# Kernel tuning notes

Measured on AMD Instinct MI355X. Metric: run time of the kernel, lower is better.

Reference implementation:

```python
import jax, jax.numpy as jnp
import numpy as np

EPS = 1e-5
NEG_SLOPE = 0.2  # torch LeakyReLU default in DGCNN-style SharedMLPs


def knn_idx(p, k):
    # p: [B, 3, N]; returns idx [B, N, k] of k nearest neighbors (incl. self)
    inner = jnp.einsum('bdn,bdm->bnm', p, p)           # [B,N,N]
    sq = jnp.sum(p * p, axis=1)                         # [B,N]
    neg_dist = 2.0 * inner - sq[:, :, None] - sq[:, None, :]
    return jax.lax.top_k(neg_dist, k)[1]                # [B,N,k]


def smlp1d(x, w, b, g, bt):
    # x: [B,C,N]; 1x1 conv + BatchNorm1d (batch stats) + LeakyReLU
    y = jnp.einsum('bcn,oc->bon', x, w) + b[None, :, None]
    m = y.mean(axis=(0, 2), keepdims=True)
    v = y.var(axis=(0, 2), keepdims=True)
    y = g[None, :, None] * (y - m) * jax.lax.rsqrt(v + EPS) + bt[None, :, None]
    return jax.nn.leaky_relu(y, NEG_SLOPE)


def edgeconv(x, idx, w, b, g, bt):
    # x: [B,C,N], idx: [B,N,k] -> [B,O,N]
    B = x.shape[0]
    xT = jnp.transpose(x, (0, 2, 1))                    # [B,N,C]
    nb = xT[jnp.arange(B)[:, None, None], idx]          # [B,N,k,C] gather
    ctr = jnp.broadcast_to(xT[:, :, None, :], nb.shape)
    feat = jnp.concatenate([nb - ctr, ctr], axis=-1)    # [B,N,k,2C]
    y = jnp.einsum('bnkc,oc->bnko', feat, w) + b        # 1x1 conv2d
    m = y.mean(axis=(0, 1, 2), keepdims=True)
    v = y.var(axis=(0, 1, 2), keepdims=True)
    y = g * (y - m) * jax.lax.rsqrt(v + EPS) + bt
    y = jax.nn.leaky_relu(y, NEG_SLOPE)
    y = jnp.max(y, axis=2)                              # max over k -> [B,N,O]
    return jnp.transpose(y, (0, 2, 1))                  # [B,O,N]


def setup_inputs() -> dict:
    key = jax.random.key(0)
    ks = jax.random.split(key, 16)
    B, N, K = 2, 8192, 20
    C_in = 1024 + 3 * 64  # emb_dims + n_edgeconvs_backbone*64 = 1216
    OUT = 50

    def lin(k, o, c):
        return jax.random.normal(k, (o, c), jnp.float32) * (1.0 / np.sqrt(c))

    return {
        'x': jax.random.normal(ks[0], (B, C_in, N), jnp.float32),
        'p': jax.random.normal(ks[1], (B, 3, N), jnp.float32),
        # smlp1: 1216 -> 256
        'w1': lin(ks[2], 256, C_in), 'b1': jnp.zeros((256,), jnp.float32),
        'g1': jnp.ones((256,), jnp.float32), 'bt1': jnp.zeros((256,), jnp.float32),
        # edgeconv: 512 -> 256
        'we': lin(ks[3], 256, 512), 'be': jnp.zeros((256,), jnp.float32),
        'ge': jnp.ones((256,), jnp.float32), 'bte': jnp.zeros((256,), jnp.float32),
        # smlp2 part 1: 256 -> 256
        'w2': lin(ks[4], 256, 256), 'b2': jnp.zeros((256,), jnp.float32),
        'g2': jnp.ones((256,), jnp.float32), 'bt2': jnp.zeros((256,), jnp.float32),
        # smlp2 part 2: 256 -> 128
        'w3': lin(ks[5], 128, 256), 'b3': jnp.zeros((128,), jnp.float32),
        'g3': jnp.ones((128,), jnp.float32), 'bt3': jnp.zeros((128,), jnp.float32),
        # final conv1d: 128 -> 50
        'wf': lin(ks[6], OUT, 128), 'bf': jnp.zeros((OUT,), jnp.float32),
    }


def reference(x, p, w1, b1, g1, bt1, we, be, ge, bte,
              w2, b2, g2, bt2, w3, b3, g3, bt3, wf, bf):
    K = 20
    h = smlp1d(x, w1, b1, g1, bt1)              # [B,256,N]
    idx = knn_idx(p, K)                          # [B,N,K]
    h = edgeconv(h, idx, we, be, ge, bte)        # [B,256,N]
    h = smlp1d(h, w2, b2, g2, bt2)               # Dropout2d: identity (eval)
    h = smlp1d(h, w3, b3, g3, bt3)               # [B,128,N]
    return jnp.einsum('bcn,oc->bon', h, wf) + bf[None, :, None]  # [B,50,N]
```

## Files before the change

kernel.cpp:

```cpp
#include <hip/hip_runtime.h>

typedef unsigned short u16;
typedef unsigned int   u32;
typedef unsigned long long u64;
typedef __attribute__((ext_vector_type(4))) float f4;
typedef __attribute__((ext_vector_type(8))) short s8;
typedef __attribute__((ext_vector_type(4))) int   i4v;
typedef __attribute__((ext_vector_type(4))) unsigned short u16x4;

#define DEV __device__ __forceinline__

DEV u16 f2b(float f) {
  u32 u = __float_as_uint(f);
  return (u16)((u + 0x7FFFu + ((u >> 16) & 1u)) >> 16);
}
DEV float b2f(u16 h) { return __uint_as_float(((u32)h) << 16); }

#define OFF_STATS 0L
#define OFF_W1B   65536L
#define OFF_WEAB  688128L
#define OFF_W2B   950272L
#define OFF_W3B   1081344L
#define OFF_IDX   1146880L
#define OFF_PQ    2457600L
#define OFF_XT    4194304L
#define OFF_Y1    44040192L
#define OFF_Y2    4194304L
#define OFF_EMAX  23068672L
#define OFF_EMIN  41943040L
#define OFF_Y3    4194304L
#define OFF_Y4    23068672L
#define WS_NEED   71303168L

__global__ __launch_bounds__(256) void k_convw(
    const float* __restrict__ w1, const float* __restrict__ we,
    const float* __restrict__ w2, const float* __restrict__ w3,
    u16* __restrict__ w1b, u16* __restrict__ weABb,
    u16* __restrict__ w2b, u16* __restrict__ w3b)
{
  int i = blockIdx.x * 256 + threadIdx.x;
  if (i < 311296) { w1b[i] = f2b(w1[i]); return; }
  i -= 311296;
  if (i < 131072) {
    int o = i >> 8, c = i & 255;
    float v = (o < 256) ? we[o * 512 + c]
                        : we[(o - 256) * 512 + 256 + c] - we[(o - 256) * 512 + c];
    weABb[i] = f2b(v); return;
  }
  i -= 131072;
  if (i < 65536) { w2b[i] = f2b(w2[i]); return; }
  i -= 65536;
  if (i < 32768) { w3b[i] = f2b(w3[i]); }
}

__global__ __launch_bounds__(256) void k_prep(const float* __restrict__ p, f4* __restrict__ pqg)
{
  int i = blockIdx.x * 256 + threadIdx.x;
  int b = i >> 13, n = i & 8191;
  const float* pb = p + (long)b * 24576;
  float X = pb[n], Y = pb[8192 + n], Z = pb[16384 + n];
  f4 v; v[0] = X; v[1] = Y; v[2] = Z; v[3] = fmaf(X, X, fmaf(Y, Y, Z * Z));
  pqg[i] = v;
}

__global__ __launch_bounds__(256) void k_xt(const float* __restrict__ x, u16* __restrict__ xt)
{
  __shared__ float t[64][65];
  const int b = blockIdx.z, ct = blockIdx.y, nt = blockIdx.x;
  const int tx = threadIdx.x & 63, ty = threadIdx.x >> 6;
  const float* xb = x + (long)b * 1216 * 8192;
#pragma unroll
  for (int i = 0; i < 16; ++i) {
    int c = ct * 64 + ty + i * 4;
    t[ty + i * 4][tx] = xb[(long)c * 8192 + nt * 64 + tx];
  }
  __syncthreads();
  u16* xtb = xt + (long)b * 8192 * 1216;
#pragma unroll
  for (int i = 0; i < 16; ++i) {
    int n = nt * 64 + ty + i * 4;
    xtb[(long)n * 1216 + ct * 64 + tx] = f2b(t[tx][ty + i * 4]);
  }
}

__global__ __launch_bounds__(256) void k_knn(const f4* __restrict__ pqg, int* __restrict__ idxOut)
{
  __shared__ f4 chunk[1024];
  __shared__ u16 cand[4][4][128];
  __shared__ double ckeyv[4][128];
  __shared__ int scnt[4][4];
  const int tid = threadIdx.x, lane = tid & 63, w = tid >> 6;
  const int blk = blockIdx.x;
  const int b = blk >> 9;
  const int qbase = ((blk & 511) << 4) + (w << 2);
  const f4* __restrict__ P = pqg + ((long)b << 13);
  if (lane < 4) scnt[w][lane] = 0;
  float qx2[4], qy2[4], qz2[4];
#pragma unroll
  for (int j = 0; j < 4; ++j) {
    f4 Q = P[qbase + j];
    qx2[j] = Q[0] + Q[0]; qy2[j] = Q[1] + Q[1]; qz2[j] = Q[2] + Q[2];
  }
  float mx[4];
#pragma unroll
  for (int j = 0; j < 4; ++j) mx[j] = -3.0e38f;
  for (int c = 0; c < 8; ++c) {
    __syncthreads();
#pragma unroll
    for (int i = 0; i < 4; ++i) chunk[tid + i * 256] = P[c * 1024 + tid + i * 256];
    __syncthreads();
#pragma unroll 2
    for (int t = 0; t < 16; ++t) {
      f4 cc = chunk[(t << 6) + lane];
#pragma unroll
      for (int j = 0; j < 4; ++j) {
        float v = fmaf(qx2[j], cc[0], fmaf(qy2[j], cc[1], fmaf(qz2[j], cc[2], -cc[3])));
        mx[j] = fmaxf(mx[j], v);
      }
    }
  }
  float sv[4];
#pragma unroll
  for (int j = 0; j < 4; ++j) sv[j] = mx[j];
#pragma unroll
  for (int k = 2; k <= 64; k <<= 1) {
#pragma unroll
    for (int s = k >> 1; s > 0; s >>= 1) {
      const bool takeMin = (((lane & k) == 0) == ((lane & s) == 0));
#pragma unroll
      for (int j = 0; j < 4; ++j) {
        float o = __shfl_xor(sv[j], s);
        sv[j] = takeMin ? fminf(sv[j], o) : fmaxf(sv[j], o);
      }
    }
  }
  float T[4];
#pragma unroll
  for (int j = 0; j < 4; ++j) T[j] = __shfl(sv[j], 44) - 1e-3f;
  for (int c = 0; c < 8; ++c) {
    __syncthreads();
#pragma unroll
    for (int i = 0; i < 4; ++i) chunk[tid + i * 256] = P[c * 1024 + tid + i * 256];
    __syncthreads();
#pragma unroll 2
    for (int t = 0; t < 16; ++t) {
      f4 cc = chunk[(t << 6) + lane];
#pragma unroll
      for (int j = 0; j < 4; ++j) {
        float v = fmaf(qx2[j], cc[0], fmaf(qy2[j], cc[1], fmaf(qz2[j], cc[2], -cc[3])));
        if (v >= T[j]) {
          int pos = atomicAdd(&scnt[w][j], 1);
          if (pos < 128) cand[w][j][pos] = (u16)(c * 1024 + (t << 6) + lane);
        }
      }
    }
  }
  asm volatile("s_waitcnt lgkmcnt(0)" ::: "memory");
  for (int j = 0; j < 4; ++j) {
    int cn = scnt[w][j]; if (cn > 128) cn = 128;
    f4 Q = P[qbase + j];
    const double Qx = (double)Q[0], Qy = (double)Q[1], Qz = (double)Q[2];
    const double Qs = Qx * Qx + Qy * Qy + Qz * Qz;
    double myV[2]; int myI[2];
#pragma unroll
    for (int jj = 0; jj < 2; ++jj) {
      const int e = lane + (jj << 6);
      myV[jj] = -1.0e300; myI[jj] = 0x7FFFFFFF;
      if (e < cn) {
        const int ci = cand[w][j][e];
        f4 c = P[ci];
        double cx = (double)c[0], cy = (double)c[1], cz = (double)c[2];
        double v = 2.0 * (Qx * cx + Qy * cy + Qz * cz) - Qs - (cx * cx + cy * cy + cz * cz);
        myV[jj] = v; myI[jj] = ci;
        ckeyv[w][e] = v;
      }
    }
    asm volatile("s_waitcnt lgkmcnt(0)" ::: "memory");
    int rk0 = 0, rk1 = 0;
#pragma unroll 4
    for (int e2 = 0; e2 < cn; ++e2) {
      double ov = ckeyv[w][e2];
      int oi = (int)cand[w][j][e2];
      rk0 += ((ov > myV[0]) || (ov == myV[0] && oi < myI[0])) ? 1 : 0;
      rk1 += ((ov > myV[1]) || (ov == myV[1] && oi < myI[1])) ? 1 : 0;
    }
    int* orow = idxOut + (((long)b << 13) + qbase + j) * 20;
    if (lane < cn && rk0 < 20) orow[rk0] = myI[0];
    if (lane + 64 < cn && rk1 < 20) orow[rk1] = myI[1];
    asm volatile("s_waitcnt lgkmcnt(0)" ::: "memory");
  }
}

DEV float lky(float z) { return z > 0.f ? z : 0.2f * z; }

DEV i4v applyPack8(f4 a, f4 b4, const float* sc, const float* sh, int kb) {
  u16 r[8];
#pragma unroll
  for (int e = 0; e < 4; ++e) r[e] = f2b(lky(fmaf(sc[kb + e], a[e], sh[kb + e])));
#pragma unroll
  for (int e = 0; e < 4; ++e) r[4 + e] = f2b(lky(fmaf(sc[kb + 4 + e], b4[e], sh[kb + 4 + e])));
  i4v o;
#pragma unroll
  for (int e = 0; e < 4; ++e) o[e] = (int)((u32)r[2 * e] | ((u32)r[2 * e + 1] << 16));
  return o;
}

DEV i4v selPack8b(i4v rawM, i4v rawN, const float* sc, const float* sh, int kb) {
  u16 r[8];
#pragma unroll
  for (int e = 0; e < 8; ++e) {
    u32 dM = (u32)rawM[e >> 1], dN = (u32)rawN[e >> 1];
    u16 hM = (e & 1) ? (u16)(dM >> 16) : (u16)(dM & 0xFFFFu);
    u16 hN = (e & 1) ? (u16)(dN >> 16) : (u16)(dN & 0xFFFFu);
    float s = sc[kb + e];
    float y = (s >= 0.f) ? b2f(hM) : b2f(hN);
    r[e] = f2b(lky(fmaf(s, y, sh[kb + e])));
  }
  i4v o;
#pragma unroll
  for (int e = 0; e < 4; ++e) o[e] = (int)((u32)r[2 * e] | ((u32)r[2 * e + 1] << 16));
  return o;
}

template<int BMODE, int STATS, int BF16OUT>
__global__ __launch_bounds__(256, 2) void k_gemm(
    const u16* __restrict__ A, const void* __restrict__ B0v, const void* __restrict__ B1v,
    const float* __restrict__ sums, const float* __restrict__ ssq,
    const float* __restrict__ g, const float* __restrict__ bt, float invCount,
    float* __restrict__ gsums, float* __restrict__ gssq,
    void* __restrict__ Yv, int M, int K, long strideB, long strideY)
{
  __shared__ u16 sA[2][4096];
  __shared__ u16 sB[2][4096];
  __shared__ float scB[256], shB[256];
  __shared__ float s_sum[128], s_ssq[128];
  const int b = blockIdx.z;
  const int m0 = blockIdx.y * 128;
  const int n0 = blockIdx.x * 128;
  const int tid = threadIdx.x, lane = tid & 63, w = tid >> 6;
  const int wr = w >> 1, wc = w & 1;
  const int r15 = lane & 15, g8 = (lane >> 4) * 8;

  if (BMODE != 0) {
    float m = sums[tid] * invCount;
    float v = ssq[tid] * invCount - m * m;
    float s = g[tid] / sqrtf(v + 1e-5f);
    scB[tid] = s;
    shB[tid] = bt[tid] - m * s;
  }
  if (STATS) { if (tid < 128) { s_sum[tid] = 0.f; s_ssq[tid] = 0.f; } }
  if (BMODE != 0) __syncthreads();

  f4 acc[4][4];
#pragma unroll
  for (int i = 0; i < 4; ++i)
#pragma unroll
    for (int j = 0; j < 4; ++j) { f4 z = {0.f, 0.f, 0.f, 0.f}; acc[i][j] = z; }

  const int row0 = tid >> 2;
  const int kp0 = (tid & 3) << 3;
  const u16* gA0 = A + (long)(m0 + row0) * K + kp0;
  const u16* gA1 = A + (long)(m0 + row0 + 64) * K + kp0;
  const int ch0 = tid, ch1 = tid + 256;

  const u16* gB0 = (const u16*)B0v + (long)b * strideB + (long)(n0 + row0) * K + kp0;
  const u16* gB1 = gB0 + (long)64 * K;
  const float* fB0 = (const float*)B0v + (long)b * strideB + (long)(n0 + row0) * K + kp0;
  const float* fB1 = fB0 + (long)64 * K;
  const u16* nB0 = (const u16*)B1v + (long)b * strideB + (long)(n0 + row0) * K + kp0;
  const u16* nB1 = nB0 + (long)64 * K;

  ((i4v*)sA[0])[ch0] = *(const i4v*)gA0;
  ((i4v*)sA[0])[ch1] = *(const i4v*)gA1;
  if (BMODE == 0) {
    ((i4v*)sB[0])[ch0] = *(const i4v*)gB0;
    ((i4v*)sB[0])[ch1] = *(const i4v*)gB1;
  } else if (BMODE == 1) {
    ((i4v*)sB[0])[ch0] = applyPack8(*(const f4*)fB0, *(const f4*)(fB0 + 4), scB, shB, kp0);
    ((i4v*)sB[0])[ch1] = applyPack8(*(const f4*)fB1, *(const f4*)(fB1 + 4), scB, shB, kp0);
  } else {
    ((i4v*)sB[0])[ch0] = selPack8b(*(const i4v*)gB0, *(const i4v*)nB0, scB, shB, kp0);
    ((i4v*)sB[0])[ch1] = selPack8b(*(const i4v*)gB1, *(const i4v*)nB1, scB, shB, kp0);
  }
  __syncthreads();

  const int KT = K >> 5;
  int cur = 0;
  for (int kk = 0; kk < KT; ++kk) {
    const bool more = (kk + 1 < KT);
    i4v ra0, ra1, rb0, rb1, rn0, rn1;
    f4 p0a, p0b, p1a, p1b;
    if (more) {
      long ko = (long)(kk + 1) * 32;
      ra0 = *(const i4v*)(gA0 + ko); ra1 = *(const i4v*)(gA1 + ko);
      if (BMODE == 0) {
        rb0 = *(const i4v*)(gB0 + ko); rb1 = *(const i4v*)(gB1 + ko);
      } else if (BMODE == 1) {
        p0a = *(const f4*)(fB0 + ko); p0b = *(const f4*)(fB0 + ko + 4);
        p1a = *(const f4*)(fB1 + ko); p1b = *(const f4*)(fB1 + ko + 4);
      } else {
        rb0 = *(const i4v*)(gB0 + ko); rb1 = *(const i4v*)(gB1 + ko);
        rn0 = *(const i4v*)(nB0 + ko); rn1 = *(const i4v*)(nB1 + ko);
      }
    }
    const u16* la = sA[cur];
    const u16* lb = sB[cur];
    s8 af[4], bfr[4];
#pragma unroll
    for (int mi = 0; mi < 4; ++mi)
      af[mi] = *(const s8*)(la + (wr * 64 + mi * 16 + r15) * 32 + g8);
#pragma unroll
    for (int ni = 0; ni < 4; ++ni)
      bfr[ni] = *(const s8*)(lb + (wc * 64 + ni * 16 + r15) * 32 + g8);
#pragma unroll
    for (int mi = 0; mi < 4; ++mi)
#pragma unroll
      for (int ni = 0; ni < 4; ++ni)
        acc[mi][ni] = __builtin_amdgcn_mfma_f32_16x16x32_bf16(af[mi], bfr[ni], acc[mi][ni], 0, 0, 0);
    if (more) {
      ((i4v*)sA[cur ^ 1])[ch0] = ra0; ((i4v*)sA[cur ^ 1])[ch1] = ra1;
      if (BMODE == 0) {
        ((i4v*)sB[cur ^ 1])[ch0] = rb0; ((i4v*)sB[cur ^ 1])[ch1] = rb1;
      } else if (BMODE == 1) {
        const int kb = (kk + 1) * 32 + kp0;
        ((i4v*)sB[cur ^ 1])[ch0] = applyPack8(p0a, p0b, scB, shB, kb);
        ((i4v*)sB[cur ^ 1])[ch1] = applyPack8(p1a, p1b, scB, shB, kb);
      } else {
        const int kb = (kk + 1) * 32 + kp0;
        ((i4v*)sB[cur ^ 1])[ch0] = selPack8b(rb0, rn0, scB, shB, kb);
        ((i4v*)sB[cur ^ 1])[ch1] = selPack8b(rb1, rn1, scB, shB, kb);
      }
    }
    __syncthreads();
    cur ^= 1;
  }
  const int og = m0 + wr * 64 + (lane >> 4) * 4;
  const int ng = n0 + wc * 64 + r15;
  if (BF16OUT) {
    u16* Yp = (u16*)Yv + (long)b * strideY;
#pragma unroll
    for (int mi = 0; mi < 4; ++mi)
#pragma unroll
      for (int ni = 0; ni < 4; ++ni) {
        f4 a = acc[mi][ni];
        u16x4 r;
#pragma unroll
        for (int q = 0; q < 4; ++q) r[q] = f2b(a[q]);
        *(u16x4*)(Yp + (long)(ng + ni * 16) * M + og + mi * 16) = r;
      }
  } else {
    float* Yp = (float*)Yv + (long)b * strideY;
#pragma unroll
    for (int mi = 0; mi < 4; ++mi)
#pragma unroll
      for (int ni = 0; ni < 4; ++ni)
        *(f4*)(Yp + (long)(ng + ni * 16) * M + og + mi * 16) = acc[mi][ni];
  }
  if (STATS) {
#pragma unroll
    for (int mi = 0; mi < 4; ++mi)
#pragma unroll
      for (int j = 0; j < 4; ++j) {
        float s = 0.f, q = 0.f;
#pragma unroll
        for (int ni = 0; ni < 4; ++ni) {
          float v = acc[mi][ni][j];
          s += v; q = fmaf(v, v, q);
        }
#pragma unroll
        for (int off = 1; off < 16; off <<= 1) {
          s += __shfl_xor(s, off);
          q += __shfl_xor(q, off);
        }
        if ((lane & 15) == 0) {
          int lc = wr * 64 + (lane >> 4) * 4 + mi * 16 + j;
          atomicAdd(&s_sum[lc], s);
          atomicAdd(&s_ssq[lc], q);
        }
      }
    __syncthreads();
    if (tid < 128) {
      atomicAdd(&gsums[m0 + tid], s_sum[tid]);
      atomicAdd(&gssq[m0 + tid], s_ssq[tid]);
    }
  }
}

__global__ __launch_bounds__(256, 2) void k_edge_gather(
    const u16* __restrict__ Y2, const int* __restrict__ idx,
    u16* __restrict__ Emax, u16* __restrict__ Emin,
    float* __restrict__ sums, float* __restrict__ ssq)
{
  __shared__ float s_sum[256], s_ssq[256];
  const int tid = threadIdx.x, lane = tid & 63, w = tid >> 6;
  s_sum[tid] = 0.f; s_ssq[tid] = 0.f;
  __syncthreads();
  const int half = blockIdx.y, b = blockIdx.z;
  const int ptBase = blockIdx.x * 64 + w * 16;
  const int sub = lane >> 5;
  const int chOff = half * 128 + ((lane & 31) << 2);
  f4 lsum = {0.f, 0.f, 0.f, 0.f}, lssq = {0.f, 0.f, 0.f, 0.f};
  for (int i = 0; i < 8; ++i) {
    const int pt = ptBase + i * 2 + sub;
    const long gp = (long)b * 8192 + pt;
    u16x4 cr = *(const u16x4*)(Y2 + gp * 512 + 256 + chOff);
    f4 ctr; ctr[0] = b2f(cr[0]); ctr[1] = b2f(cr[1]); ctr[2] = b2f(cr[2]); ctr[3] = b2f(cr[3]);
    const int* irow = idx + gp * 20;
    f4 vmax = {-3.0e38f, -3.0e38f, -3.0e38f, -3.0e38f};
    f4 vmin = {3.0e38f, 3.0e38f, 3.0e38f, 3.0e38f};
#pragma unroll 4
    for (int k = 0; k < 20; ++k) {
      int m = irow[k];
      u16x4 nr = *(const u16x4*)(Y2 + ((long)b * 8192 + m) * 512 + chOff);
#pragma unroll
      for (int j = 0; j < 4; ++j) {
        float y = b2f(nr[j]) + ctr[j];
        vmax[j] = fmaxf(vmax[j], y);
        vmin[j] = fminf(vmin[j], y);
        lsum[j] += y;
        lssq[j] = fmaf(y, y, lssq[j]);
      }
    }
    u16x4 eM, eN;
#pragma unroll
    for (int j = 0; j < 4; ++j) { eM[j] = f2b(vmax[j]); eN[j] = f2b(vmin[j]); }
    *(u16x4*)(Emax + gp * 256 + chOff) = eM;
    *(u16x4*)(Emin + gp * 256 + chOff) = eN;
  }
#pragma unroll
  for (int j = 0; j < 4; ++j) {
    atomicAdd(&s_sum[chOff + j], lsum[j]);
    atomicAdd(&s_ssq[chOff + j], lssq[j]);
  }
  __syncthreads();
  atomicAdd(&sums[tid], s_sum[tid]);
  atomicAdd(&ssq[tid], s_ssq[tid]);
}

__global__ __launch_bounds__(64) void k_final(
    const float* __restrict__ Y4, const float* __restrict__ sums, const float* __restrict__ ssq,
    const float* __restrict__ g, const float* __restrict__ bt,
    const float* __restrict__ wf, const float* __restrict__ bf,
    float* __restrict__ out)
{
  __shared__ float swf[128][56];
  __shared__ float sc[128], sh[128], sb[52];
  const int lane = threadIdx.x;
  if (lane < 50) {
    const float* wrow = wf + lane * 128;
#pragma unroll 8
    for (int ch = 0; ch < 128; ++ch) swf[ch][lane] = wrow[ch];
    sb[lane] = bf[lane];
  } else if (lane < 52) {
#pragma unroll 8
    for (int ch = 0; ch < 128; ++ch) swf[ch][lane] = 0.f;
    sb[lane] = 0.f;
  }
#pragma unroll
  for (int t = 0; t < 2; ++t) {
    int ch = lane + t * 64;
    float m = sums[ch] * (1.0f / 16384.0f);
    float v = ssq[ch] * (1.0f / 16384.0f) - m * m;
    float s = g[ch] / sqrtf(v + 1e-5f);
    sc[ch] = s;
    sh[ch] = bt[ch] - m * s;
  }
  __syncthreads();
  const int b = blockIdx.y;
  const int n = blockIdx.x * 64 + lane;
  const float* hp = Y4 + ((long)b * 8192 + n) * 128;
  f4 av[13];
#pragma unroll
  for (int i = 0; i < 13; ++i) { f4 z = {0.f, 0.f, 0.f, 0.f}; av[i] = z; }
#pragma unroll 4
  for (int c4 = 0; c4 < 32; ++c4) {
    f4 hv = *(const f4*)(hp + c4 * 4);
#pragma unroll
    for (int e = 0; e < 4; ++e) {
      const int ch = c4 * 4 + e;
      float z = lky(fmaf(sc[ch], hv[e], sh[ch]));
#pragma unroll
      for (int o4 = 0; o4 < 13; ++o4) {
        f4 wv = *(const f4*)&swf[ch][o4 * 4];
#pragma unroll
        for (int q = 0; q < 4; ++q) av[o4][q] = fmaf(z, wv[q], av[o4][q]);
      }
    }
  }
  float* ob = out + (((long)b * 50) << 13) + n;
#pragma unroll
  for (int o4 = 0; o4 < 13; ++o4)
#pragma unroll
    for (int q = 0; q < 4; ++q) {
      int o = o4 * 4 + q;
      if (o < 50) ob[(long)o << 13] = av[o4][q] + sb[o];
    }
}

extern "C" void kernel_launch(void* const* d_in, const int* in_sizes, int n_in,
                              void* d_out, int out_size, void* d_ws, size_t ws_size,
                              hipStream_t stream)
{
  if ((long)ws_size < WS_NEED) return;
  const float* x   = (const float*)d_in[0];
  const float* p   = (const float*)d_in[1];
  const float* w1  = (const float*)d_in[2];
  const float* g1w = (const float*)d_in[4];
  const float* bt1 = (const float*)d_in[5];
  const float* we  = (const float*)d_in[6];
  const float* gew = (const float*)d_in[8];
  const float* bte = (const float*)d_in[9];
  const float* w2  = (const float*)d_in[10];
  const float* g2w = (const float*)d_in[12];
  const float* bt2 = (const float*)d_in[13];
  const float* w3  = (const float*)d_in[14];
  const float* g3w = (const float*)d_in[16];
  const float* bt3 = (const float*)d_in[17];
  const float* wf  = (const float*)d_in[18];
  const float* bfi = (const float*)d_in[19];

  char* ws = (char*)d_ws;
  u16* w1b   = (u16*)(ws + OFF_W1B);
  u16* weABb = (u16*)(ws + OFF_WEAB);
  u16* w2b   = (u16*)(ws + OFF_W2B);
  u16* w3b   = (u16*)(ws + OFF_W3B);
  int* idxb  = (int*)(ws + OFF_IDX);
  f4*  pqg   = (f4*)(ws + OFF_PQ);
  u16*   XT   = (u16*)(ws + OFF_XT);
  float* Y1   = (float*)(ws + OFF_Y1);
  u16*   Y2b  = (u16*)(ws + OFF_Y2);
  u16*   EMAX = (u16*)(ws + OFF_EMAX);
  u16*   EMIN = (u16*)(ws + OFF_EMIN);
  float* Y3   = (float*)(ws + OFF_Y3);
  float* Y4   = (float*)(ws + OFF_Y4);
  float* st0 = (float*)(ws + OFF_STATS);
  float* st1 = (float*)(ws + OFF_STATS + 4096);
  float* st2 = (float*)(ws + OFF_STATS + 8192);
  float* st3 = (float*)(ws + OFF_STATS + 12288);

  hipMemsetAsync(ws + OFF_STATS, 0, 16384, stream);
  k_convw<<<2112, 256, 0, stream>>>(w1, we, w2, w3, w1b, weABb, w2b, w3b);
  k_prep<<<64, 256, 0, stream>>>(p, pqg);
  k_knn<<<1024, 256, 0, stream>>>(pqg, idxb);
  k_xt<<<dim3(128, 19, 2), 256, 0, stream>>>(x, XT);

  k_gemm<0, 1, 0><<<dim3(64, 2, 2), 256, 0, stream>>>(
      w1b, XT, nullptr, nullptr, nullptr, nullptr, nullptr, 0.f,
      st0, st0 + 256, Y1, 256, 1216, (long)8192 * 1216, (long)8192 * 256);

  k_gemm<1, 0, 1><<<dim3(64, 4, 2), 256, 0, stream>>>(
      weABb, Y1, nullptr, st0, st0 + 256, g1w, bt1, 1.0f / 16384.0f,
      nullptr, nullptr, Y2b, 512, 256, (long)8192 * 256, (long)8192 * 512);

  k_edge_gather<<<dim3(128, 2, 2), 256, 0, stream>>>(Y2b, idxb, EMAX, EMIN, st1, st1 + 256);

  k_gemm<2, 1, 0><<<dim3(64, 2, 2), 256, 0, stream>>>(
      w2b, EMAX, EMIN, st1, st1 + 256, gew, bte, 1.0f / 327680.0f,
      st2, st2 + 256, Y3, 256, 256, (long)8192 * 256, (long)8192 * 256);

  k_gemm<1, 1, 0><<<dim3(64, 1, 2), 256, 0, stream>>>(
      w3b, Y3, nullptr, st2, st2 + 256, g2w, bt2, 1.0f / 16384.0f,
      st3, st3 + 256, Y4, 128, 256, (long)8192 * 256, (long)8192 * 128);

  k_final<<<dim3(128, 2), 64, 0, stream>>>(Y4, st3, st3 + 256, g3w, bt3, wf, bfi, (float*)d_out);
}
```

Before: 235.5 us.

## Fuse x transpose/bf16 conversion into first GEMM and merge prep into weight conversion

```diff
diff --git a/kernel.cpp b/kernel.cpp
--- a/kernel.cpp
+++ b/kernel.cpp
@@ -23,7 +23,6 @@
 #define OFF_W3B   1081344L
 #define OFF_IDX   1146880L
 #define OFF_PQ    2457600L
-#define OFF_XT    4194304L
 #define OFF_Y1    44040192L
 #define OFF_Y2    4194304L
 #define OFF_EMAX  23068672L
@@ -35,8 +34,9 @@
 __global__ __launch_bounds__(256) void k_convw(
     const float* __restrict__ w1, const float* __restrict__ we,
     const float* __restrict__ w2, const float* __restrict__ w3,
+    const float* __restrict__ p,
     u16* __restrict__ w1b, u16* __restrict__ weABb,
-    u16* __restrict__ w2b, u16* __restrict__ w3b)
+    u16* __restrict__ w2b, u16* __restrict__ w3b, f4* __restrict__ pqg)
 {
   int i = blockIdx.x * 256 + threadIdx.x;
   if (i < 311296) { w1b[i] = f2b(w1[i]); return; }
@@ -50,36 +50,14 @@
   i -= 131072;
   if (i < 65536) { w2b[i] = f2b(w2[i]); return; }
   i -= 65536;
-  if (i < 32768) { w3b[i] = f2b(w3[i]); }
-}
-
-__global__ __launch_bounds__(256) void k_prep(const float* __restrict__ p, f4* __restrict__ pqg)
-{
-  int i = blockIdx.x * 256 + threadIdx.x;
-  int b = i >> 13, n = i & 8191;
-  const float* pb = p + (long)b * 24576;
-  float X = pb[n], Y = pb[8192 + n], Z = pb[16384 + n];
-  f4 v; v[0] = X; v[1] = Y; v[2] = Z; v[3] = fmaf(X, X, fmaf(Y, Y, Z * Z));
-  pqg[i] = v;
-}
-
-__global__ __launch_bounds__(256) void k_xt(const float* __restrict__ x, u16* __restrict__ xt)
-{
-  __shared__ float t[64][65];
-  const int b = blockIdx.z, ct = blockIdx.y, nt = blockIdx.x;
-  const int tx = threadIdx.x & 63, ty = threadIdx.x >> 6;
-  const float* xb = x + (long)b * 1216 * 8192;
-#pragma unroll
-  for (int i = 0; i < 16; ++i) {
-    int c = ct * 64 + ty + i * 4;
-    t[ty + i * 4][tx] = xb[(long)c * 8192 + nt * 64 + tx];
-  }
-  __syncthreads();
-  u16* xtb = xt + (long)b * 8192 * 1216;
-#pragma unroll
-  for (int i = 0; i < 16; ++i) {
-    int n = nt * 64 + ty + i * 4;
-    xtb[(long)n * 1216 + ct * 64 + tx] = f2b(t[tx][ty + i * 4]);
+  if (i < 32768) { w3b[i] = f2b(w3[i]); return; }
+  i -= 32768;
+  if (i < 16384) {
+    int b = i >> 13, n = i & 8191;
+    const float* pb = p + (long)b * 24576;
+    float X = pb[n], Y = pb[8192 + n], Z = pb[16384 + n];
+    f4 v; v[0] = X; v[1] = Y; v[2] = Z; v[3] = fmaf(X, X, fmaf(Y, Y, Z * Z));
+    pqg[i] = v;
   }
 }
 
@@ -222,6 +200,14 @@
   return o;
 }
 
+#define XSTRIDE 130
+DEV s8 packFrag(const float* __restrict__ sBf, int kb, int nl) {
+  union { u16 u[8]; s8 v; } r;
+#pragma unroll
+  for (int i = 0; i < 8; ++i) r.u[i] = f2b(sBf[(kb + i) * XSTRIDE + nl]);
+  return r.v;
+}
+
 template<int BMODE, int STATS, int BF16OUT>
 __global__ __launch_bounds__(256, 2) void k_gemm(
     const u16* __restrict__ A, const void* __restrict__ B0v, const void* __restrict__ B1v,
@@ -231,7 +217,7 @@
     void* __restrict__ Yv, int M, int K, long strideB, long strideY)
 {
   __shared__ u16 sA[2][4096];
-  __shared__ u16 sB[2][4096];
+  __shared__ __align__(16) char sBr[2][(BMODE == 3) ? 16640 : 8192];
   __shared__ float scB[256], shB[256];
   __shared__ float s_sum[128], s_ssq[128];
   const int b = blockIdx.z;
@@ -241,7 +227,7 @@
   const int wr = w >> 1, wc = w & 1;
   const int r15 = lane & 15, g8 = (lane >> 4) * 8;
 
-  if (BMODE != 0) {
+  if (BMODE == 1 || BMODE == 2) {
     float m = sums[tid] * invCount;
     float v = ssq[tid] * invCount - m * m;
     float s = g[tid] / sqrtf(v + 1e-5f);
@@ -249,7 +235,7 @@
     shB[tid] = bt[tid] - m * s;
   }
   if (STATS) { if (tid < 128) { s_sum[tid] = 0.f; s_ssq[tid] = 0.f; } }
-  if (BMODE != 0) __syncthreads();
+  if (BMODE == 1 || BMODE == 2) __syncthreads();
 
   f4 acc[4][4];
 #pragma unroll
@@ -269,18 +255,30 @@
   const float* fB1 = fB0 + (long)64 * K;
   const u16* nB0 = (const u16*)B1v + (long)b * strideB + (long)(n0 + row0) * K + kp0;
   const u16* nB1 = nB0 + (long)64 * K;
+  const float* xB = (const float*)B0v + (long)b * strideB;
+  const int kS = tid >> 3, nS = (tid & 7) << 2;
+  const float* gX = xB + (long)kS * 8192 + n0 + nS;
 
   ((i4v*)sA[0])[ch0] = *(const i4v*)gA0;
   ((i4v*)sA[0])[ch1] = *(const i4v*)gA1;
   if (BMODE == 0) {
-    ((i4v*)sB[0])[ch0] = *(const i4v*)gB0;
-    ((i4v*)sB[0])[ch1] = *(const i4v*)gB1;
+    ((i4v*)sBr[0])[ch0] = *(const i4v*)gB0;
+    ((i4v*)sBr[0])[ch1] = *(const i4v*)gB1;
   } else if (BMODE == 1) {
-    ((i4v*)sB[0])[ch0] = applyPack8(*(const f4*)fB0, *(const f4*)(fB0 + 4), scB, shB, kp0);
-    ((i4v*)sB[0])[ch1] = applyPack8(*(const f4*)fB1, *(const f4*)(fB1 + 4), scB, shB, kp0);
+    ((i4v*)sBr[0])[ch0] = applyPack8(*(const f4*)fB0, *(const f4*)(fB0 + 4), scB, shB, kp0);
+    ((i4v*)sBr[0])[ch1] = applyPack8(*(const f4*)fB1, *(const f4*)(fB1 + 4), scB, shB, kp0);
+  } else if (BMODE == 2) {
+    ((i4v*)sBr[0])[ch0] = selPack8b(*(const i4v*)gB0, *(const i4v*)nB0, scB, shB, kp0);
+    ((i4v*)sBr[0])[ch1] = selPack8b(*(const i4v*)gB1, *(const i4v*)nB1, scB, shB, kp0);
   } else {
-    ((i4v*)sB[0])[ch0] = selPack8b(*(const i4v*)gB0, *(const i4v*)nB0, scB, shB, kp0);
-    ((i4v*)sB[0])[ch1] = selPack8b(*(const i4v*)gB1, *(const i4v*)nB1, scB, shB, kp0);
+    float* sBf0 = (float*)sBr[0];
+#pragma unroll
+    for (int it = 0; it < 4; ++it) {
+      f4 v = *(const f4*)(gX + it * 32);
+      float* dst = sBf0 + kS * XSTRIDE + nS + it * 32;
+      ((float2*)dst)[0] = make_float2(v[0], v[1]);
+      ((float2*)dst)[1] = make_float2(v[2], v[3]);
+    }
   }
   __syncthreads();
 
@@ -290,6 +288,7 @@
     const bool more = (kk + 1 < KT);
     i4v ra0, ra1, rb0, rb1, rn0, rn1;
     f4 p0a, p0b, p1a, p1b;
+    f4 xv[4];
     if (more) {
       long ko = (long)(kk + 1) * 32;
       ra0 = *(const i4v*)(gA0 + ko); ra1 = *(const i4v*)(gA1 + ko);
@@ -298,20 +297,31 @@
       } else if (BMODE == 1) {
         p0a = *(const f4*)(fB0 + ko); p0b = *(const f4*)(fB0 + ko + 4);
         p1a = *(const f4*)(fB1 + ko); p1b = *(const f4*)(fB1 + ko + 4);
-      } else {
+      } else if (BMODE == 2) {
         rb0 = *(const i4v*)(gB0 + ko); rb1 = *(const i4v*)(gB1 + ko);
         rn0 = *(const i4v*)(nB0 + ko); rn1 = *(const i4v*)(nB1 + ko);
+      } else {
+        const float* gx = gX + ko * 8192;
+#pragma unroll
+        for (int it = 0; it < 4; ++it) xv[it] = *(const f4*)(gx + it * 32);
       }
     }
     const u16* la = sA[cur];
-    const u16* lb = sB[cur];
     s8 af[4], bfr[4];
 #pragma unroll
     for (int mi = 0; mi < 4; ++mi)
       af[mi] = *(const s8*)(la + (wr * 64 + mi * 16 + r15) * 32 + g8);
-#pragma unroll
-    for (int ni = 0; ni < 4; ++ni)
-      bfr[ni] = *(const s8*)(lb + (wc * 64 + ni * 16 + r15) * 32 + g8);
+    if (BMODE == 3) {
+      const float* sBfc = (const float*)sBr[cur];
+#pragma unroll
+      for (int ni = 0; ni < 4; ++ni)
+        bfr[ni] = packFrag(sBfc, g8, wc * 64 + ni * 16 + r15);
+    } else {
+      const u16* lb = (const u16*)sBr[cur];
+#pragma unroll
+      for (int ni = 0; ni < 4; ++ni)
+        bfr[ni] = *(const s8*)(lb + (wc * 64 + ni * 16 + r15) * 32 + g8);
+    }
 #pragma unroll
     for (int mi = 0; mi < 4; ++mi)
 #pragma unroll
@@ -320,15 +330,23 @@
     if (more) {
       ((i4v*)sA[cur ^ 1])[ch0] = ra0; ((i4v*)sA[cur ^ 1])[ch1] = ra1;
       if (BMODE == 0) {
-        ((i4v*)sB[cur ^ 1])[ch0] = rb0; ((i4v*)sB[cur ^ 1])[ch1] = rb1;
+        ((i4v*)sBr[cur ^ 1])[ch0] = rb0; ((i4v*)sBr[cur ^ 1])[ch1] = rb1;
       } else if (BMODE == 1) {
         const int kb = (kk + 1) * 32 + kp0;
-        ((i4v*)sB[cur ^ 1])[ch0] = applyPack8(p0a, p0b, scB, shB, kb);
-        ((i4v*)sB[cur ^ 1])[ch1] = applyPack8(p1a, p1b, scB, shB, kb);
+        ((i4v*)sBr[cur ^ 1])[ch0] = applyPack8(p0a, p0b, scB, shB, kb);
+        ((i4v*)sBr[cur ^ 1])[ch1] = applyPack8(p1a, p1b, scB, shB, kb);
+      } else if (BMODE == 2) {
+        const int kb = (kk + 1) * 32 + kp0;
+        ((i4v*)sBr[cur ^ 1])[ch0] = selPack8b(rb0, rn0, scB, shB, kb);
+        ((i4v*)sBr[cur ^ 1])[ch1] = selPack8b(rb1, rn1, scB, shB, kb);
       } else {
-        const int kb = (kk + 1) * 32 + kp0;
-        ((i4v*)sB[cur ^ 1])[ch0] = selPack8b(rb0, rn0, scB, shB, kb);
-        ((i4v*)sB[cur ^ 1])[ch1] = selPack8b(rb1, rn1, scB, shB, kb);
+        float* sBfn = (float*)sBr[cur ^ 1];
+#pragma unroll
+        for (int it = 0; it < 4; ++it) {
+          float* dst = sBfn + kS * XSTRIDE + nS + it * 32;
+          ((float2*)dst)[0] = make_float2(xv[it][0], xv[it][1]);
+          ((float2*)dst)[1] = make_float2(xv[it][2], xv[it][3]);
+        }
       }
     }
     __syncthreads();
@@ -526,7 +544,6 @@
   u16* w3b   = (u16*)(ws + OFF_W3B);
   int* idxb  = (int*)(ws + OFF_IDX);
   f4*  pqg   = (f4*)(ws + OFF_PQ);
-  u16*   XT   = (u16*)(ws + OFF_XT);
   float* Y1   = (float*)(ws + OFF_Y1);
   u16*   Y2b  = (u16*)(ws + OFF_Y2);
   u16*   EMAX = (u16*)(ws + OFF_EMAX);
@@ -539,14 +556,12 @@
   float* st3 = (float*)(ws + OFF_STATS + 12288);
 
   hipMemsetAsync(ws + OFF_STATS, 0, 16384, stream);
-  k_convw<<<2112, 256, 0, stream>>>(w1, we, w2, w3, w1b, weABb, w2b, w3b);
-  k_prep<<<64, 256, 0, stream>>>(p, pqg);
+  k_convw<<<2176, 256, 0, stream>>>(w1, we, w2, w3, p, w1b, weABb, w2b, w3b, pqg);
   k_knn<<<1024, 256, 0, stream>>>(pqg, idxb);
-  k_xt<<<dim3(128, 19, 2), 256, 0, stream>>>(x, XT);
-
-  k_gemm<0, 1, 0><<<dim3(64, 2, 2), 256, 0, stream>>>(
-      w1b, XT, nullptr, nullptr, nullptr, nullptr, nullptr, 0.f,
-      st0, st0 + 256, Y1, 256, 1216, (long)8192 * 1216, (long)8192 * 256);
+
+  k_gemm<3, 1, 0><<<dim3(64, 2, 2), 256, 0, stream>>>(
+      w1b, x, nullptr, nullptr, nullptr, nullptr, nullptr, 0.f,
+      st0, st0 + 256, Y1, 256, 1216, (long)1216 * 8192, (long)8192 * 256);
 
   k_gemm<1, 0, 1><<<dim3(64, 4, 2), 256, 0, stream>>>(
       weABb, Y1, nullptr, st0, st0 + 256, g1w, bt1, 1.0f / 16384.0f,
```

New measurement: 223.0 us. 1.06x faster.
